# Kernel optimization log

Hardware: AMD Instinct MI355X
Metric: run time of the kernel (lower is better)

Reference implementation:

```python
import jax, jax.numpy as jnp
import numpy as np

EPS = 1e-5
SLOPE = 0.01  # torch LeakyReLU default


def _bn(h, gamma, beta):
    # BatchNorm1d in training mode: biased batch stats over dim 0
    m = jnp.mean(h, axis=0)
    v = jnp.var(h, axis=0)
    return (h - m) * jax.lax.rsqrt(v + EPS) * gamma + beta


def _leaky(h):
    return jnp.where(h >= 0, h, SLOPE * h)


def _xavier(key, fan_in, fan_out):
    lim = np.sqrt(6.0 / (fan_in + fan_out))
    return jax.random.uniform(key, (fan_in, fan_out), jnp.float32, -lim, lim)


def setup_inputs() -> dict:
    key = jax.random.key(0)
    ks = jax.random.split(key, 12)
    N, E, B = 50000, 800000, 500
    D_NODE, D_EDGE, HID, OUT = 64, 64, 128, 128
    x = jax.random.normal(ks[0], (N, D_NODE), jnp.float32)
    edge_index = jax.random.randint(ks[1], (2, E), 0, N, jnp.int64)
    edge_attr = jax.random.normal(ks[2], (E, D_EDGE), jnp.float32)
    u = jnp.zeros((B, 1), jnp.float32)
    batch = jnp.sort(jax.random.randint(ks[3], (N,), 0, B, jnp.int64))
    b = lambda n: jnp.full((n,), 0.01, jnp.float32)
    return {
        "x": x, "edge_index": edge_index, "edge_attr": edge_attr, "u": u, "batch": batch,
        # global_mlp_1: Lin(128,128) LeakyReLU BN Lin(128,128)
        "W1a": _xavier(ks[4], D_NODE + D_EDGE, HID), "b1a": b(HID),
        "g1a": jnp.ones((HID,), jnp.float32), "be1a": jnp.zeros((HID,), jnp.float32),
        "W2a": _xavier(ks[5], HID, HID), "b2a": b(HID),
        # global_mlp_2: Lin(192,128) LReLU BN Lin(128,128) LReLU BN Lin(128,128)
        "W1b": _xavier(ks[6], HID + D_NODE, HID), "b1b": b(HID),
        "g1b": jnp.ones((HID,), jnp.float32), "be1b": jnp.zeros((HID,), jnp.float32),
        "W2b": _xavier(ks[7], HID, HID), "b2b": b(HID),
        "g2b": jnp.ones((HID,), jnp.float32), "be2b": jnp.zeros((HID,), jnp.float32),
        "W3b": _xavier(ks[8], HID, OUT), "b3b": b(OUT),
    }


def reference(x, edge_index, edge_attr, u, batch,
              W1a, b1a, g1a, be1a, W2a, b2a,
              W1b, b1b, g1b, be1b, W2b, b2b, g2b, be2b, W3b, b3b):
    N = x.shape[0]
    B = u.shape[0]
    row, col = edge_index[0], edge_index[1]
    # gather source nodes, concat edge features -> edge MLP
    h = jnp.concatenate([x[row], edge_attr], axis=1)          # [E, 128]
    h = _bn(_leaky(h @ W1a + b1a), g1a, be1a) @ W2a + b2a     # [E, hid]
    # scatter_add edges -> destination nodes
    node_agg = jax.ops.segment_sum(h, col, num_segments=N)    # [N, hid]
    # per-graph sums
    gx = jax.ops.segment_sum(x, batch, num_segments=B)        # [B, 64]
    ga = jax.ops.segment_sum(node_agg, batch, num_segments=B) # [B, hid]
    g = jnp.concatenate([gx, ga], axis=1)                     # [B, 192]
    g = _bn(_leaky(g @ W1b + b1b), g1b, be1b)
    g = _bn(_leaky(g @ W2b + b2b), g2b, be2b)
    return g @ W3b + b3b                                      # [B, 128]
```

## Files before the change

kernel.cpp:

```cpp
#include <hip/hip_runtime.h>

#define EPS 1e-5f
#define SLOPE 0.01f
#define NBMAX 512

typedef __attribute__((ext_vector_type(8))) short bf16x8;
typedef __attribute__((ext_vector_type(4))) float f32x4;
typedef __attribute__((ext_vector_type(4))) short s16x4;

__device__ __forceinline__ float leaky(float z) { return z >= 0.f ? z : SLOPE * z; }

__device__ __forceinline__ short f2bf(float f) {
    unsigned u = __float_as_uint(f);
    u += 0x7fff + ((u >> 16) & 1);
    return (short)(u >> 16);
}

__global__ __launch_bounds__(256) void k_prep(
    const float* __restrict__ x, short* __restrict__ xb,
    const float* __restrict__ W1a, short* __restrict__ WT,
    const int* __restrict__ ei, const int* __restrict__ batch,
    int* __restrict__ gdst, int* __restrict__ counts, int* __restrict__ node_off,
    int N, int E, int B, int nbx, int nbh, int nbn) {
    __shared__ int h[NBMAX];
    const int bid = blockIdx.x, t = threadIdx.x;
    if (bid < nbx) {
        int i = bid * 256 + t;
        if (i < N * 16) {
            f32x4 v = ((const f32x4*)x)[i];
            s16x4 o;
#pragma unroll
            for (int j = 0; j < 4; ++j) o[j] = f2bf(v[j]);
            ((s16x4*)xb)[i] = o;
        }
    } else if (bid < nbx + nbh) {
        for (int b = t; b < NBMAX; b += 256) h[b] = 0;
        __syncthreads();
        int base = (bid - nbx) * 4096;
#pragma unroll
        for (int i = 0; i < 16; ++i) {
            int e = base + i * 256 + t;
            if (e < E) {
                int g = batch[ei[E + e]];
                gdst[e] = g;
                atomicAdd(&h[g], 1);
            }
        }
        __syncthreads();
        for (int b = t; b < NBMAX; b += 256)
            if (h[b]) atomicAdd(&counts[b], h[b]);
    } else if (bid < nbx + nbh + nbn) {
        int n = (bid - nbx - nbh) * 256 + t;
        if (n < N) {
            int b1 = batch[n];
            int prev = (n == 0) ? -1 : batch[n - 1];
            for (int g = prev + 1; g <= b1; ++g) node_off[g] = n;
            if (n == N - 1)
                for (int g = b1 + 1; g <= B; ++g) node_off[g] = N;
        }
    } else {
        int c = t >> 1, k0 = (t & 1) * 64;
        for (int k = 0; k < 64; ++k)
            WT[c * 128 + k0 + k] = f2bf(W1a[(k0 + k) * 128 + c]);
    }
}

__global__ void k_scan(const int* __restrict__ counts, int* __restrict__ edge_off,
                       int* __restrict__ cursor, int B) {
    __shared__ int s[1024];
    int t = threadIdx.x;
    s[t] = (t < B) ? counts[t] : 0;
    __syncthreads();
    for (int d = 1; d < 1024; d <<= 1) {
        int v = (t >= d) ? s[t - d] : 0;
        __syncthreads();
        s[t] += v;
        __syncthreads();
    }
    if (t <= B) {
        int excl = (t == 0) ? 0 : s[t - 1];
        edge_off[t] = excl;
        if (t < B) cursor[t] = excl;
    }
}

__global__ __launch_bounds__(256) void k_pos(const int* __restrict__ gdst,
                                             int* __restrict__ cursor,
                                             int* __restrict__ pos_g, int E) {
    __shared__ int cnt[NBMAX];
    __shared__ int basep[NBMAX];
    int t = threadIdx.x;
    for (int b = t; b < NBMAX; b += 256) cnt[b] = 0;
    __syncthreads();
    int blk = blockIdx.x * 4096;
    int g[16], rk[16];
#pragma unroll
    for (int i = 0; i < 16; ++i) {
        int e = blk + i * 256 + t;
        g[i] = (e < E) ? gdst[e] : -1;
        rk[i] = (g[i] >= 0) ? atomicAdd(&cnt[g[i]], 1) : 0;
    }
    __syncthreads();
    for (int b = t; b < NBMAX; b += 256) {
        int c = cnt[b];
        basep[b] = c ? atomicAdd(&cursor[b], c) : 0;
    }
    __syncthreads();
#pragma unroll
    for (int i = 0; i < 16; ++i)
        if (g[i] >= 0) pos_g[blk + i * 256 + t] = basep[g[i]] + rk[i];
}

__global__ __launch_bounds__(256) void k_gather(
    const float* __restrict__ ea, const short* __restrict__ xb,
    const int* __restrict__ ei, const int* __restrict__ pos_g,
    short* __restrict__ As, const float* __restrict__ x,
    const int* __restrict__ node_off, float* __restrict__ gx, int E, int nbg) {
    const int bid = blockIdx.x;
    const int lane = threadIdx.x & 63, wave = threadIdx.x >> 6;
    if (bid < nbg) {
        int r = lane >> 4, c16 = lane & 15;
        int base = bid * 1024;
#pragma unroll 4
        for (int eb = wave * 4; eb < 1024; eb += 16) {
            int e = base + eb + r;
            if (e < E) {
                int rid = ei[e];
                int p = pos_g[e];
                s16x4 xv = *(const s16x4*)(xb + (size_t)rid * 64 + c16 * 4);
                f32x4 v = *(const f32x4*)(ea + (size_t)e * 64 + c16 * 4);
                s16x4 o;
#pragma unroll
                for (int j = 0; j < 4; ++j) o[j] = f2bf(v[j]);
                short* dst = As + (size_t)p * 128;
                *(s16x4*)(dst + c16 * 4) = xv;
                *(s16x4*)(dst + 64 + c16 * 4) = o;
            }
        }
    } else {
        __shared__ float part[4][64];
        int g = bid - nbg;
        int n0 = node_off[g], n1 = node_off[g + 1];
        float a = 0.f;
        for (int n = n0 + wave; n < n1; n += 4) a += x[(size_t)n * 64 + lane];
        part[wave][lane] = a;
        __syncthreads();
        if (wave == 0)
            gx[g * 64 + lane] =
                (part[0][lane] + part[1][lane]) + (part[2][lane] + part[3][lane]);
    }
}

__global__ __launch_bounds__(256, 2) void k_edges(
    const short* __restrict__ As, const int* __restrict__ edge_off,
    const short* __restrict__ WT, const float* __restrict__ b1a,
    float* __restrict__ Sg, float* __restrict__ Qg, int CH) {
    const int g = blockIdx.x;
    const int lane = threadIdx.x & 63, wave = threadIdx.x >> 6;
    const int m = lane & 15, quad = lane >> 4;

    bf16x8 Wf[4][8];
#pragma unroll
    for (int t = 0; t < 8; ++t)
#pragma unroll
        for (int ks = 0; ks < 4; ++ks)
            Wf[ks][t] = *(const bf16x8*)(WT + (t * 16 + m) * 128 + ks * 32 + quad * 8);
    float bb[8];
#pragma unroll
    for (int t = 0; t < 8; ++t) bb[t] = b1a[t * 16 + m];

    const int e0 = edge_off[g], e1 = edge_off[g + 1];
    const int cnt = e1 - e0;
    const int chunk = (cnt + CH - 1) / CH;
    const int lo = e0 + blockIdx.y * chunk;
    const int hi = min(lo + chunk, e1);

    float accS[8] = {0, 0, 0, 0, 0, 0, 0, 0};
    float accQ[8] = {0, 0, 0, 0, 0, 0, 0, 0};

    for (int ib = lo + wave * 16; ib < hi; ib += 64) {
        int idx = min(ib + m, hi - 1);
        const short* arow = As + (size_t)idx * 128;
        bf16x8 A0 = *(const bf16x8*)(arow + quad * 8);
        bf16x8 A1 = *(const bf16x8*)(arow + 32 + quad * 8);
        bf16x8 A2 = *(const bf16x8*)(arow + 64 + quad * 8);
        bf16x8 A3 = *(const bf16x8*)(arow + 96 + quad * 8);
        float vf[4];
#pragma unroll
        for (int r2 = 0; r2 < 4; ++r2) vf[r2] = ((ib + quad * 4 + r2) < hi) ? 1.f : 0.f;
#pragma unroll
        for (int t = 0; t < 8; ++t) {
            f32x4 c = {0.f, 0.f, 0.f, 0.f};
            c = __builtin_amdgcn_mfma_f32_16x16x32_bf16(A0, Wf[0][t], c, 0, 0, 0);
            c = __builtin_amdgcn_mfma_f32_16x16x32_bf16(A1, Wf[1][t], c, 0, 0, 0);
            c = __builtin_amdgcn_mfma_f32_16x16x32_bf16(A2, Wf[2][t], c, 0, 0, 0);
            c = __builtin_amdgcn_mfma_f32_16x16x32_bf16(A3, Wf[3][t], c, 0, 0, 0);
#pragma unroll
            for (int r2 = 0; r2 < 4; ++r2) {
                float z = c[r2] + bb[t];
                float a = fmaf(SLOPE, fminf(z, 0.f), fmaxf(z, 0.f)) * vf[r2];
                accS[t] += a;
                accQ[t] = fmaf(a, a, accQ[t]);
            }
        }
    }
#pragma unroll
    for (int t = 0; t < 8; ++t) {
        float s = accS[t];
        s += __shfl_xor(s, 16);
        s += __shfl_xor(s, 32);
        float q = accQ[t];
        q += __shfl_xor(q, 16);
        q += __shfl_xor(q, 32);
        if (quad == 0) {
            atomicAdd(&Sg[g * 128 + t * 16 + m], s);
            atomicAdd(&Qg[g * 128 + t * 16 + m], q);
        }
    }
}

__global__ __launch_bounds__(128) void k_stats_part(const float* __restrict__ Sg,
                                                    const float* __restrict__ Qg,
                                                    float* __restrict__ Stot,
                                                    float* __restrict__ Qtot, int B) {
    int c = threadIdx.x;
    int per = (B + gridDim.x - 1) / gridDim.x;
    int g0 = blockIdx.x * per, g1 = min(g0 + per, B);
    float S = 0.f, Q = 0.f;
    for (int g = g0; g < g1; ++g) {
        S += Sg[g * 128 + c];
        Q += Qg[g * 128 + c];
    }
    atomicAdd(&Stot[c], S);
    atomicAdd(&Qtot[c], Q);
}

__global__ __launch_bounds__(128) void k_g1(
    const float* __restrict__ Sg, const float* __restrict__ Stot,
    const float* __restrict__ Qtot, const float* __restrict__ gx,
    const int* __restrict__ edge_off, const float* __restrict__ g1a,
    const float* __restrict__ be1a, const float* __restrict__ W2a,
    const float* __restrict__ b2a, const float* __restrict__ W1b,
    const float* __restrict__ b1b, float* __restrict__ a1,
    float* __restrict__ sum1, float* __restrict__ sumsq1, float invE) {
    __shared__ float T[128];
    __shared__ float gcat[192];
    int g = blockIdx.x, c = threadIdx.x;
    float mn = Stot[c] * invE;
    float v = Qtot[c] * invE - mn * mn;
    float sc = g1a[c] * rsqrtf(v + EPS);
    float sh = be1a[c] - mn * sc;
    float cg = (float)(edge_off[g + 1] - edge_off[g]);
    T[c] = Sg[g * 128 + c] * sc + cg * sh;
    if (c < 64) gcat[c] = gx[g * 64 + c];
    __syncthreads();
    float ga = cg * b2a[c];
#pragma unroll 8
    for (int k = 0; k < 128; ++k) ga = fmaf(T[k], W2a[k * 128 + c], ga);
    gcat[64 + c] = ga;
    __syncthreads();
    float z = b1b[c];
#pragma unroll 8
    for (int k = 0; k < 192; ++k) z = fmaf(gcat[k], W1b[k * 128 + c], z);
    float av = leaky(z);
    a1[g * 128 + c] = av;
    atomicAdd(&sum1[c], av);
    atomicAdd(&sumsq1[c], av * av);
}

__global__ __launch_bounds__(128) void k_bn_lin(
    const float* __restrict__ a_prev, const float* __restrict__ sum,
    const float* __restrict__ sumsq, const float* __restrict__ gma,
    const float* __restrict__ bta, const float* __restrict__ W,
    const float* __restrict__ b, float* __restrict__ a_out,
    float* __restrict__ sum_out, float* __restrict__ sumsq_out, float invB,
    int do_leaky) {
    __shared__ float hs[128];
    int g = blockIdx.x, c = threadIdx.x;
    float mn = sum[c] * invB;
    float v = sumsq[c] * invB - mn * mn;
    float sc = gma[c] * rsqrtf(v + EPS);
    float sh = bta[c] - mn * sc;
    hs[c] = a_prev[g * 128 + c] * sc + sh;
    __syncthreads();
    float z = b[c];
#pragma unroll 8
    for (int k = 0; k < 128; ++k) z = fmaf(hs[k], W[k * 128 + c], z);
    if (do_leaky) {
        z = leaky(z);
        a_out[g * 128 + c] = z;
        atomicAdd(&sum_out[c], z);
        atomicAdd(&sumsq_out[c], z * z);
    } else {
        a_out[g * 128 + c] = z;
    }
}

extern "C" void kernel_launch(void* const* d_in, const int* in_sizes, int n_in,
                              void* d_out, int out_size, void* d_ws, size_t ws_size,
                              hipStream_t stream) {
    const float* x    = (const float*)d_in[0];
    const int*   ei   = (const int*)d_in[1];
    const float* ea   = (const float*)d_in[2];
    const int*   batch= (const int*)d_in[4];
    const float* W1a  = (const float*)d_in[5];
    const float* b1a  = (const float*)d_in[6];
    const float* g1a  = (const float*)d_in[7];
    const float* be1a = (const float*)d_in[8];
    const float* W2a  = (const float*)d_in[9];
    const float* b2a  = (const float*)d_in[10];
    const float* W1b  = (const float*)d_in[11];
    const float* b1b  = (const float*)d_in[12];
    const float* g1b  = (const float*)d_in[13];
    const float* be1b = (const float*)d_in[14];
    const float* W2b  = (const float*)d_in[15];
    const float* b2b  = (const float*)d_in[16];
    const float* g2b  = (const float*)d_in[17];
    const float* be2b = (const float*)d_in[18];
    const float* W3b  = (const float*)d_in[19];
    const float* b3b  = (const float*)d_in[20];

    const int N = in_sizes[0] / 64;
    const int E = in_sizes[1] / 2;
    const int B = in_sizes[3];

    char* ws = (char*)d_ws;
    size_t off = 0;
    auto alloc = [&](size_t bytes) -> char* {
        char* p = ws + off;
        off = (off + bytes + 255) & ~(size_t)255;
        return p;
    };
    int*   counts = (int*)alloc((size_t)B * 4);
    float* Sg     = (float*)alloc((size_t)B * 128 * 4);
    float* Qg     = (float*)alloc((size_t)B * 128 * 4);
    float* sum1   = (float*)alloc(128 * 4);
    float* sumsq1 = (float*)alloc(128 * 4);
    float* sum2   = (float*)alloc(128 * 4);
    float* sumsq2 = (float*)alloc(128 * 4);
    float* Stot   = (float*)alloc(128 * 4);
    float* Qtot   = (float*)alloc(128 * 4);
    size_t zbytes = off;
    short* xb      = (short*)alloc((size_t)N * 64 * 2);
    short* WT      = (short*)alloc(128 * 128 * 2);
    int*   gdst    = (int*)alloc((size_t)E * 4);
    int*   pos_g   = (int*)alloc((size_t)E * 4);
    short* As      = (short*)alloc((size_t)E * 128 * 2);
    int*   edge_off= (int*)alloc((size_t)(B + 1) * 4);
    int*   cursor  = (int*)alloc((size_t)B * 4);
    int*   node_off= (int*)alloc((size_t)(B + 1) * 4);
    float* gx      = (float*)alloc((size_t)B * 64 * 4);
    float* a1      = (float*)alloc((size_t)B * 128 * 4);
    float* a2      = (float*)alloc((size_t)B * 128 * 4);
    (void)ws_size;
    (void)n_in;

    hipMemsetAsync(ws, 0, zbytes, stream);

    const int nbx = (N * 16 + 255) / 256;
    const int nbh = (E + 4095) / 4096;
    const int nbn = (N + 255) / 256;
    k_prep<<<dim3(nbx + nbh + nbn + 1), dim3(256), 0, stream>>>(
        x, xb, W1a, WT, ei, batch, gdst, counts, node_off, N, E, B, nbx, nbh, nbn);
    k_scan<<<dim3(1), dim3(1024), 0, stream>>>(counts, edge_off, cursor, B);
    k_pos<<<dim3(nbh), dim3(256), 0, stream>>>(gdst, cursor, pos_g, E);
    const int nbg = (E + 1023) / 1024;
    k_gather<<<dim3(nbg + B), dim3(256), 0, stream>>>(ea, xb, ei, pos_g, As, x,
                                                      node_off, gx, E, nbg);
    const int CH = 8;
    k_edges<<<dim3(B, CH), dim3(256), 0, stream>>>(As, edge_off, WT, b1a, Sg, Qg, CH);
    k_stats_part<<<dim3(25), dim3(128), 0, stream>>>(Sg, Qg, Stot, Qtot, B);
    k_g1<<<dim3(B), dim3(128), 0, stream>>>(Sg, Stot, Qtot, gx, edge_off, g1a, be1a,
                                            W2a, b2a, W1b, b1b, a1, sum1, sumsq1,
                                            1.0f / (float)E);
    k_bn_lin<<<dim3(B), dim3(128), 0, stream>>>(a1, sum1, sumsq1, g1b, be1b, W2b,
                                                b2b, a2, sum2, sumsq2,
                                                1.0f / (float)B, 1);
    k_bn_lin<<<dim3(B), dim3(128), 0, stream>>>(a2, sum2, sumsq2, g2b, be2b, W3b,
                                                b3b, (float*)d_out, nullptr, nullptr,
                                                1.0f / (float)B, 0);
}
```

Before: 580.9 us.

## Gather edge rows inside MFMA kernel instead of materializing sorted bf16 buffer

```diff
diff --git a/kernel.cpp b/kernel.cpp
--- a/kernel.cpp
+++ b/kernel.cpp
@@ -14,6 +14,20 @@
     unsigned u = __float_as_uint(f);
     u += 0x7fff + ((u >> 16) & 1);
     return (short)(u >> 16);
+}
+
+__device__ __forceinline__ unsigned pack2(float f0, float f1) {
+    unsigned u0 = __float_as_uint(f0) + 0x8000u;
+    unsigned u1 = __float_as_uint(f1) + 0x8000u;
+    return __builtin_amdgcn_perm(u1, u0, 0x07060302u);
+}
+__device__ __forceinline__ bf16x8 pack8(f32x4 lo, f32x4 hi) {
+    union { bf16x8 v; unsigned u[4]; } r;
+    r.u[0] = pack2(lo[0], lo[1]);
+    r.u[1] = pack2(lo[2], lo[3]);
+    r.u[2] = pack2(hi[0], hi[1]);
+    r.u[3] = pack2(hi[2], hi[3]);
+    return r.v;
 }
 
 __global__ __launch_bounds__(256) void k_prep(
@@ -84,62 +98,44 @@
     }
 }
 
-__global__ __launch_bounds__(256) void k_pos(const int* __restrict__ gdst,
-                                             int* __restrict__ cursor,
-                                             int* __restrict__ pos_g, int E) {
+__global__ __launch_bounds__(256) void k_pos(
+    const int* __restrict__ gdst, const int* __restrict__ ei,
+    int* __restrict__ cursor, int* __restrict__ perm, int* __restrict__ rows_s,
+    const float* __restrict__ x, const int* __restrict__ node_off,
+    float* __restrict__ gx, int E, int nbh) {
     __shared__ int cnt[NBMAX];
     __shared__ int basep[NBMAX];
-    int t = threadIdx.x;
-    for (int b = t; b < NBMAX; b += 256) cnt[b] = 0;
-    __syncthreads();
-    int blk = blockIdx.x * 4096;
-    int g[16], rk[16];
-#pragma unroll
-    for (int i = 0; i < 16; ++i) {
-        int e = blk + i * 256 + t;
-        g[i] = (e < E) ? gdst[e] : -1;
-        rk[i] = (g[i] >= 0) ? atomicAdd(&cnt[g[i]], 1) : 0;
-    }
-    __syncthreads();
-    for (int b = t; b < NBMAX; b += 256) {
-        int c = cnt[b];
-        basep[b] = c ? atomicAdd(&cursor[b], c) : 0;
-    }
-    __syncthreads();
-#pragma unroll
-    for (int i = 0; i < 16; ++i)
-        if (g[i] >= 0) pos_g[blk + i * 256 + t] = basep[g[i]] + rk[i];
-}
-
-__global__ __launch_bounds__(256) void k_gather(
-    const float* __restrict__ ea, const short* __restrict__ xb,
-    const int* __restrict__ ei, const int* __restrict__ pos_g,
-    short* __restrict__ As, const float* __restrict__ x,
-    const int* __restrict__ node_off, float* __restrict__ gx, int E, int nbg) {
-    const int bid = blockIdx.x;
-    const int lane = threadIdx.x & 63, wave = threadIdx.x >> 6;
-    if (bid < nbg) {
-        int r = lane >> 4, c16 = lane & 15;
-        int base = bid * 1024;
-#pragma unroll 4
-        for (int eb = wave * 4; eb < 1024; eb += 16) {
-            int e = base + eb + r;
-            if (e < E) {
-                int rid = ei[e];
-                int p = pos_g[e];
-                s16x4 xv = *(const s16x4*)(xb + (size_t)rid * 64 + c16 * 4);
-                f32x4 v = *(const f32x4*)(ea + (size_t)e * 64 + c16 * 4);
-                s16x4 o;
-#pragma unroll
-                for (int j = 0; j < 4; ++j) o[j] = f2bf(v[j]);
-                short* dst = As + (size_t)p * 128;
-                *(s16x4*)(dst + c16 * 4) = xv;
-                *(s16x4*)(dst + 64 + c16 * 4) = o;
+    __shared__ float part[4][64];
+    const int bid = blockIdx.x, t = threadIdx.x;
+    if (bid < nbh) {
+        for (int b = t; b < NBMAX; b += 256) cnt[b] = 0;
+        __syncthreads();
+        int blk = bid * 4096;
+        int g[16], rk[16];
+#pragma unroll
+        for (int i = 0; i < 16; ++i) {
+            int e = blk + i * 256 + t;
+            g[i] = (e < E) ? gdst[e] : -1;
+            rk[i] = (g[i] >= 0) ? atomicAdd(&cnt[g[i]], 1) : 0;
+        }
+        __syncthreads();
+        for (int b = t; b < NBMAX; b += 256) {
+            int c = cnt[b];
+            basep[b] = c ? atomicAdd(&cursor[b], c) : 0;
+        }
+        __syncthreads();
+#pragma unroll
+        for (int i = 0; i < 16; ++i) {
+            int e = blk + i * 256 + t;
+            if (g[i] >= 0) {
+                int pos = basep[g[i]] + rk[i];
+                perm[pos] = e;
+                rows_s[pos] = ei[e];
             }
         }
     } else {
-        __shared__ float part[4][64];
-        int g = bid - nbg;
+        int g = bid - nbh;
+        int lane = t & 63, wave = t >> 6;
         int n0 = node_off[g], n1 = node_off[g + 1];
         float a = 0.f;
         for (int n = n0 + wave; n < n1; n += 4) a += x[(size_t)n * 64 + lane];
@@ -151,10 +147,12 @@
     }
 }
 
-__global__ __launch_bounds__(256, 2) void k_edges(
-    const short* __restrict__ As, const int* __restrict__ edge_off,
-    const short* __restrict__ WT, const float* __restrict__ b1a,
-    float* __restrict__ Sg, float* __restrict__ Qg, int CH) {
+__global__ __launch_bounds__(256) void k_edges2(
+    const short* __restrict__ xb, const float* __restrict__ ea,
+    const int* __restrict__ rows_s, const int* __restrict__ perm,
+    const int* __restrict__ edge_off, const short* __restrict__ WT,
+    const float* __restrict__ b1a, float* __restrict__ Sg, float* __restrict__ Qg,
+    int CH) {
     const int g = blockIdx.x;
     const int lane = threadIdx.x & 63, wave = threadIdx.x >> 6;
     const int m = lane & 15, quad = lane >> 4;
@@ -180,27 +178,53 @@
 
     for (int ib = lo + wave * 16; ib < hi; ib += 64) {
         int idx = min(ib + m, hi - 1);
-        const short* arow = As + (size_t)idx * 128;
-        bf16x8 A0 = *(const bf16x8*)(arow + quad * 8);
-        bf16x8 A1 = *(const bf16x8*)(arow + 32 + quad * 8);
-        bf16x8 A2 = *(const bf16x8*)(arow + 64 + quad * 8);
-        bf16x8 A3 = *(const bf16x8*)(arow + 96 + quad * 8);
-        float vf[4];
-#pragma unroll
-        for (int r2 = 0; r2 < 4; ++r2) vf[r2] = ((ib + quad * 4 + r2) < hi) ? 1.f : 0.f;
-#pragma unroll
-        for (int t = 0; t < 8; ++t) {
-            f32x4 c = {0.f, 0.f, 0.f, 0.f};
-            c = __builtin_amdgcn_mfma_f32_16x16x32_bf16(A0, Wf[0][t], c, 0, 0, 0);
-            c = __builtin_amdgcn_mfma_f32_16x16x32_bf16(A1, Wf[1][t], c, 0, 0, 0);
-            c = __builtin_amdgcn_mfma_f32_16x16x32_bf16(A2, Wf[2][t], c, 0, 0, 0);
-            c = __builtin_amdgcn_mfma_f32_16x16x32_bf16(A3, Wf[3][t], c, 0, 0, 0);
-#pragma unroll
-            for (int r2 = 0; r2 < 4; ++r2) {
-                float z = c[r2] + bb[t];
-                float a = fmaf(SLOPE, fminf(z, 0.f), fmaxf(z, 0.f)) * vf[r2];
-                accS[t] += a;
-                accQ[t] = fmaf(a, a, accQ[t]);
+        int rid = rows_s[idx];
+        int e = perm[idx];
+        const short* xr = xb + (size_t)rid * 64;
+        bf16x8 A0 = *(const bf16x8*)(xr + quad * 8);
+        bf16x8 A1 = *(const bf16x8*)(xr + 32 + quad * 8);
+        const float* er = ea + (size_t)e * 64;
+        f32x4 p0 = *(const f32x4*)(er + quad * 8);
+        f32x4 p1 = *(const f32x4*)(er + quad * 8 + 4);
+        f32x4 p2 = *(const f32x4*)(er + 32 + quad * 8);
+        f32x4 p3 = *(const f32x4*)(er + 32 + quad * 8 + 4);
+        bf16x8 A2 = pack8(p0, p1);
+        bf16x8 A3 = pack8(p2, p3);
+        if (ib + 16 <= hi) {
+#pragma unroll
+            for (int t = 0; t < 8; ++t) {
+                f32x4 c = {0.f, 0.f, 0.f, 0.f};
+                c = __builtin_amdgcn_mfma_f32_16x16x32_bf16(A0, Wf[0][t], c, 0, 0, 0);
+                c = __builtin_amdgcn_mfma_f32_16x16x32_bf16(A1, Wf[1][t], c, 0, 0, 0);
+                c = __builtin_amdgcn_mfma_f32_16x16x32_bf16(A2, Wf[2][t], c, 0, 0, 0);
+                c = __builtin_amdgcn_mfma_f32_16x16x32_bf16(A3, Wf[3][t], c, 0, 0, 0);
+#pragma unroll
+                for (int r2 = 0; r2 < 4; ++r2) {
+                    float z = c[r2] + bb[t];
+                    float a = fmaf(SLOPE, fminf(z, 0.f), fmaxf(z, 0.f));
+                    accS[t] += a;
+                    accQ[t] = fmaf(a, a, accQ[t]);
+                }
+            }
+        } else {
+            float vf[4];
+#pragma unroll
+            for (int r2 = 0; r2 < 4; ++r2)
+                vf[r2] = ((ib + quad * 4 + r2) < hi) ? 1.f : 0.f;
+#pragma unroll
+            for (int t = 0; t < 8; ++t) {
+                f32x4 c = {0.f, 0.f, 0.f, 0.f};
+                c = __builtin_amdgcn_mfma_f32_16x16x32_bf16(A0, Wf[0][t], c, 0, 0, 0);
+                c = __builtin_amdgcn_mfma_f32_16x16x32_bf16(A1, Wf[1][t], c, 0, 0, 0);
+                c = __builtin_amdgcn_mfma_f32_16x16x32_bf16(A2, Wf[2][t], c, 0, 0, 0);
+                c = __builtin_amdgcn_mfma_f32_16x16x32_bf16(A3, Wf[3][t], c, 0, 0, 0);
+#pragma unroll
+                for (int r2 = 0; r2 < 4; ++r2) {
+                    float z = c[r2] + bb[t];
+                    float a = fmaf(SLOPE, fminf(z, 0.f), fmaxf(z, 0.f)) * vf[r2];
+                    accS[t] += a;
+                    accQ[t] = fmaf(a, a, accQ[t]);
+                }
             }
         }
     }
@@ -344,8 +368,8 @@
     short* xb      = (short*)alloc((size_t)N * 64 * 2);
     short* WT      = (short*)alloc(128 * 128 * 2);
     int*   gdst    = (int*)alloc((size_t)E * 4);
-    int*   pos_g   = (int*)alloc((size_t)E * 4);
-    short* As      = (short*)alloc((size_t)E * 128 * 2);
+    int*   perm    = (int*)alloc((size_t)E * 4);
+    int*   rows_s  = (int*)alloc((size_t)E * 4);
     int*   edge_off= (int*)alloc((size_t)(B + 1) * 4);
     int*   cursor  = (int*)alloc((size_t)B * 4);
     int*   node_off= (int*)alloc((size_t)(B + 1) * 4);
@@ -363,12 +387,11 @@
     k_prep<<<dim3(nbx + nbh + nbn + 1), dim3(256), 0, stream>>>(
         x, xb, W1a, WT, ei, batch, gdst, counts, node_off, N, E, B, nbx, nbh, nbn);
     k_scan<<<dim3(1), dim3(1024), 0, stream>>>(counts, edge_off, cursor, B);
-    k_pos<<<dim3(nbh), dim3(256), 0, stream>>>(gdst, cursor, pos_g, E);
-    const int nbg = (E + 1023) / 1024;
-    k_gather<<<dim3(nbg + B), dim3(256), 0, stream>>>(ea, xb, ei, pos_g, As, x,
-                                                      node_off, gx, E, nbg);
-    const int CH = 8;
-    k_edges<<<dim3(B, CH), dim3(256), 0, stream>>>(As, edge_off, WT, b1a, Sg, Qg, CH);
+    k_pos<<<dim3(nbh + B), dim3(256), 0, stream>>>(gdst, ei, cursor, perm, rows_s,
+                                                   x, node_off, gx, E, nbh);
+    const int CH = 2;
+    k_edges2<<<dim3(B, CH), dim3(256), 0, stream>>>(xb, ea, rows_s, perm, edge_off,
+                                                    WT, b1a, Sg, Qg, CH);
     k_stats_part<<<dim3(25), dim3(128), 0, stream>>>(Sg, Qg, Stot, Qtot, B);
     k_g1<<<dim3(B), dim3(128), 0, stream>>>(Sg, Stot, Qtot, gx, edge_off, g1a, be1a,
                                             W2a, b2a, W1b, b1b, a1, sum1, sumsq1,
```

After: 481.7 us. -17.1%, faster.
